# Kernel tuning notes

Measured on AMD Instinct MI355X. Metric: run time of the kernel, lower is better.

Reference implementation:

```python
import jax, jax.numpy as jnp
import numpy as np

# AdEx constants (from source module)
T_REF = 2e-3
CM = 281e-12
GL = 30e-9
EL = -70.6e-3
VT = -50.4e-3
DELTAT = 2e-3
TAUW = 144e-3
A = 4e-9
B = 0.0805e-9
DT = 1e-3
REF_STEPS = int(round(T_REF / DT))  # 2 steps


def setup_inputs() -> dict:
    key = jax.random.key(0)
    T, N = 500, 100000
    # input current ~ nanoamps so a fraction of neurons spike
    I = jax.random.normal(key, (T, N), dtype=jnp.float32) * 0.5e-9 + 0.5e-9
    v0 = jnp.full((N,), EL, dtype=jnp.float32)      # membrane potential at rest
    c0 = jnp.zeros((N,), dtype=jnp.float32)         # adaptation variable
    ref0 = jnp.zeros((N,), dtype=jnp.int32)         # refractory counters
    return {"I": I, "v0": v0, "c0": c0, "ref0": ref0}


def reference(I, v0, c0, ref0):
    """AdEx neuron simulation: scan over T timesteps, [N] state vectors.
    Returns v_trace of shape [T, N]."""

    def step(carry, I_t):
        v, c, ref = carry
        in_ref = ref > 0
        # refractory neurons are clamped to EL (tf.where(ref_op, EL, v))
        v_eff = jnp.where(in_ref, EL, v)
        # AdEx membrane dynamics (forward Euler); exp arg clipped for safety
        exp_term = GL * DELTAT * jnp.exp(jnp.minimum((v_eff - VT) / DELTAT, 15.0))
        dv = (DT / CM) * (-GL * (v_eff - EL) + exp_term - c + I_t)
        v_new = jnp.where(in_ref, EL, v_eff + dv)
        # adaptation current dynamics
        c_new = c + (DT / TAUW) * (A * (v_eff - EL) - c)
        # spike detection + reset
        spike = v_new >= VT
        v_out = jnp.where(spike, EL, v_new)
        c_out = jnp.where(spike, c_new + B, c_new)
        ref_new = jnp.where(spike, REF_STEPS, jnp.maximum(ref - 1, 0))
        return (v_out, c_out, ref_new), v_out

    (_, _, _), v_trace = jax.lax.scan(step, (v0, c0, ref0), I)
    return v_trace
```

## Files before the change

### kernel.cpp

```cpp
#include <hip/hip_runtime.h>


#define DEPTH 24

__global__ __launch_bounds__(64) void adex_kernel(
    const float* __restrict__ I,
    const float* __restrict__ v0,
    const float* __restrict__ c0,
    const int*   __restrict__ ref0,
    float*       __restrict__ out,
    int N, int T)
{
#pragma clang fp contract(off)
    const float EL       = (float)(-70.6e-3);
    const float VT       = (float)(-50.4e-3);
    const float DELTAT   = (float)(2e-3);
    const float R_DELTAT = (float)(1.0 / (double)((float)(2e-3)));
    const float NEG_GL   = (float)(-30e-9);
    const float GLDT     = (float)(30e-9 * 2e-3);
    const float DT_CM    = (float)(1e-3 / 281e-12);
    const float DT_TAUW  = (float)(1e-3 / 144e-3);
    const float Af       = (float)(4e-9);
    const float Bf       = (float)(0.0805e-9);
    const int   REF_STEPS = 2;

    int n = blockIdx.x * blockDim.x + threadIdx.x;
    if (n >= N) return;

    float v  = v0[n];
    float c  = c0[n];
    int   rf = ref0[n];

    const unsigned stride_b = (unsigned)N * 4u;

    auto step = [&](float It) -> float {
        bool  in_ref = rf > 0;
        float v_eff  = in_ref ? EL : v;

        float x   = v_eff - VT;
        float y0  = x * R_DELTAT;
        float e   = fmaf(-DELTAT, y0, x);
        float arg = fmaf(e, R_DELTAT, y0);
        arg = fminf(arg, 15.0f);
        float exp_term = GLDT * expf(arg);

        float acc = NEG_GL * (v_eff - EL);
        acc = acc + exp_term;
        acc = acc - c;
        acc = acc + It;
        float dv = DT_CM * acc;

        float v_new = in_ref ? EL : (v_eff + dv);
        float c_new = c + DT_TAUW * ((Af * (v_eff - EL)) - c);

        bool  spike = v_new >= VT;
        float v_out = spike ? EL : v_new;

        c  = spike ? (c_new + Bf) : c_new;
        rf = spike ? REF_STEPS : (in_ref ? rf - 1 : 0);
        v  = v_out;
        return v_out;
    };

    unsigned off = (unsigned)n * 4u;

    if (T >= 2 * DEPTH) {
        const char* Ip = (const char*)I + (size_t)DEPTH * (size_t)stride_b;

        float buf[DEPTH];
        {
            unsigned poff = off;
#pragma unroll
            for (int k = 0; k < DEPTH; ++k) {
                buf[k] = *(const float*)((const char*)I + poff);
                poff += stride_b;
            }
        }

        int t = 0;
        for (; t + 2 * DEPTH <= T; t += DEPTH) {
#pragma unroll
            for (int j = 0; j < DEPTH; ++j) {
                float It = buf[j];
                buf[j] = *(const float*)(Ip + off);
                float v_out = step(It);
                __builtin_nontemporal_store(v_out, (float*)((char*)out + off));
                off += stride_b;
            }
        }

#pragma unroll
        for (int j = 0; j < 2 * DEPTH; ++j) {
            if (t + j < T) {
                float It = buf[j % DEPTH];
                if (t + j + DEPTH < T) {
                    buf[j % DEPTH] = *(const float*)(Ip + off);
                }
                float v_out = step(It);
                __builtin_nontemporal_store(v_out, (float*)((char*)out + off));
                off += stride_b;
            }
        }
    } else {
        for (int tt = 0; tt < T; ++tt) {
            float It = *(const float*)((const char*)I + off);
            float v_out = step(It);
            __builtin_nontemporal_store(v_out, (float*)((char*)out + off));
            off += stride_b;
        }
    }
}

extern "C" void kernel_launch(void* const* d_in, const int* in_sizes, int n_in,
                              void* d_out, int out_size, void* d_ws, size_t ws_size,
                              hipStream_t stream) {
    const float* I    = (const float*)d_in[0];
    const float* v0   = (const float*)d_in[1];
    const float* c0   = (const float*)d_in[2];
    const int*   ref0 = (const int*)d_in[3];
    float*       out  = (float*)d_out;

    int N = in_sizes[1];
    int T = in_sizes[0] / N;

    dim3 block(64);
    dim3 grid((N + 63) / 64);
    adex_kernel<<<grid, block, 0, stream>>>(I, v0, c0, ref0, out, N, T);
}
```

Measured before the change: 363.7 us.

## Stage input tiles into LDS via async global_load_lds with double buffering

Input loads move from a per-thread register prefetch ring to 16-byte global_load_lds transfers into two LDS tiles of 32 timesteps. The next tile streams in while the current one is simulated, and the kernel reads LDS through a small register ring, synchronising with manual vmcnt waits. Partial blocks are split into a separate template path with clamped addresses. The aim is fewer VGPRs and wider, more latency-tolerant loads, but the hand-written waitcnt relies on counting outstanding memory ops (including stores) and could race or over-wait.

```diff
diff --git a/kernel.cpp b/kernel.cpp
--- a/kernel.cpp
+++ b/kernel.cpp
@@ -1,15 +1,27 @@
 #include <hip/hip_runtime.h>
 
 
-#define DEPTH 24
+#define TS 32
 
-__global__ __launch_bounds__(64) void adex_kernel(
+__device__ __forceinline__ void stage16(const void* g, void* l) {
+    __builtin_amdgcn_global_load_lds(
+        (const __attribute__((address_space(1))) void*)g,
+        (__attribute__((address_space(3))) void*)l, 16, 0, 0);
+}
+__device__ __forceinline__ void stage4(const void* g, void* l) {
+    __builtin_amdgcn_global_load_lds(
+        (const __attribute__((address_space(1))) void*)g,
+        (__attribute__((address_space(3))) void*)l, 4, 0, 0);
+}
+
+template <bool FULL>
+__device__ __forceinline__ void run_sim(
     const float* __restrict__ I,
     const float* __restrict__ v0,
     const float* __restrict__ c0,
     const int*   __restrict__ ref0,
     float*       __restrict__ out,
-    int N, int T)
+    int N, int T, float* bufA, float* bufB)
 {
 #pragma clang fp contract(off)
     const float EL       = (float)(-70.6e-3);
@@ -24,14 +36,19 @@
     const float Bf       = (float)(0.0805e-9);
     const int   REF_STEPS = 2;
 
-    int n = blockIdx.x * blockDim.x + threadIdx.x;
-    if (n >= N) return;
+    const int lane   = threadIdx.x;
+    const int n_base = blockIdx.x * 64;
+    const int n      = n_base + lane;
+    const bool active = FULL || (n < N);
+    const int  nld    = FULL ? n : (n < N ? n : N - 1);
 
-    float v  = v0[n];
-    float c  = c0[n];
-    int   rf = ref0[n];
+    float v  = v0[nld];
+    float c  = c0[nld];
+    int   rf = ref0[nld];
 
     const unsigned stride_b = (unsigned)N * 4u;
+    const char* Ic = (const char*)I;
+    char*       oc = (char*)out;
 
     auto step = [&](float It) -> float {
         bool  in_ref = rf > 0;
@@ -62,52 +79,84 @@
         return v_out;
     };
 
+    int col16 = n_base * 4 + (lane & 15) * 16;
+    if (!FULL) { int mx = N * 4 - 16; col16 = col16 < mx ? col16 : mx; }
+    const char* gst = Ic + (size_t)(lane >> 4) * stride_b + (size_t)col16;
+
+    int col4 = n * 4;
+    if (!FULL) { int mx = N * 4 - 4; col4 = col4 < mx ? col4 : mx; }
+
     unsigned off = (unsigned)n * 4u;
 
-    if (T >= 2 * DEPTH) {
-        const char* Ip = (const char*)I + (size_t)DEPTH * (size_t)stride_b;
+    const int nt = (T + TS - 1) / TS;
 
-        float buf[DEPTH];
-        {
-            unsigned poff = off;
-#pragma unroll
-            for (int k = 0; k < DEPTH; ++k) {
-                buf[k] = *(const float*)((const char*)I + poff);
-                poff += stride_b;
+    auto stage_tile = [&](int k, float* sb) {
+        int t0   = k * TS;
+        int rows = T - t0; if (rows > TS) rows = TS;
+        int full = rows >> 2;
+        for (int i = 0; i < full; ++i) {
+            stage16(gst, sb + i * 256);
+            gst += 4 * (size_t)stride_b;
+        }
+        int rem = rows & 3;
+        if (rem) {
+            const char* g4 = Ic + (size_t)(t0 + (full << 2)) * stride_b + (size_t)col4;
+            float* lb = sb + (full << 2) * 64;
+            for (int r = 0; r < rem; ++r) {
+                stage4(g4, lb);
+                g4 += stride_b; lb += 64;
             }
         }
+    };
 
-        int t = 0;
-        for (; t + 2 * DEPTH <= T; t += DEPTH) {
+    auto tile_body = [&](int k, const float* rb, float* sb) {
+        if (k + 1 < nt) stage_tile(k + 1, sb);
+
+        int rows = T - k * TS; if (rows > TS) rows = TS;
+
+        float ring[4];
 #pragma unroll
-            for (int j = 0; j < DEPTH; ++j) {
-                float It = buf[j];
-                buf[j] = *(const float*)(Ip + off);
+        for (int i = 0; i < 4; ++i)
+            if (i < rows) ring[i] = rb[i * 64 + lane];
+
+#pragma unroll
+        for (int r = 0; r < TS; ++r) {
+            if (r < rows) {
+                float It = ring[r & 3];
+                if (r + 4 < rows) ring[r & 3] = rb[(r + 4) * 64 + lane];
                 float v_out = step(It);
-                __builtin_nontemporal_store(v_out, (float*)((char*)out + off));
+                if (active)
+                    __builtin_nontemporal_store(v_out, (float*)(oc + off));
                 off += stride_b;
             }
         }
+        asm volatile("s_waitcnt vmcnt(32)" ::: "memory");
+    };
 
-#pragma unroll
-        for (int j = 0; j < 2 * DEPTH; ++j) {
-            if (t + j < T) {
-                float It = buf[j % DEPTH];
-                if (t + j + DEPTH < T) {
-                    buf[j % DEPTH] = *(const float*)(Ip + off);
-                }
-                float v_out = step(It);
-                __builtin_nontemporal_store(v_out, (float*)((char*)out + off));
-                off += stride_b;
-            }
-        }
+    stage_tile(0, bufA);
+    asm volatile("s_waitcnt vmcnt(0)" ::: "memory");
+
+    for (int k = 0; k < nt; k += 2) {
+        tile_body(k, bufA, bufB);
+        if (k + 1 < nt) tile_body(k + 1, bufB, bufA);
+    }
+}
+
+__global__ __launch_bounds__(64) void adex_kernel(
+    const float* __restrict__ I,
+    const float* __restrict__ v0,
+    const float* __restrict__ c0,
+    const int*   __restrict__ ref0,
+    float*       __restrict__ out,
+    int N, int T)
+{
+    __shared__ float bufA[TS * 64];
+    __shared__ float bufB[TS * 64];
+
+    if (blockIdx.x * 64 + 64 <= (unsigned)N) {
+        run_sim<true >(I, v0, c0, ref0, out, N, T, bufA, bufB);
     } else {
-        for (int tt = 0; tt < T; ++tt) {
-            float It = *(const float*)((const char*)I + off);
-            float v_out = step(It);
-            __builtin_nontemporal_store(v_out, (float*)((char*)out + off));
-            off += stride_b;
-        }
+        run_sim<false>(I, v0, c0, ref0, out, N, T, bufA, bufB);
     }
 }
 
```

New measurement: 400.4 us. +10.1%, slower.

## Double-buffer input prefetch in 32-step chunks with sched barriers

Applied to the files above, without the earlier changes.

Replaces the rolling 24-deep per-step prefetch ring with two 32-element register buffers that alternate. Each chunk of loads is issued ahead of the matching compute block, and scheduling barriers stop the compiler from interleaving them. It also switches from nontemporal stores to plain stores. The intent is deeper, batched memory-level parallelism, at the cost of more register use and extra predicated tail logic.

```diff
diff --git a/kernel.cpp b/kernel.cpp
--- a/kernel.cpp
+++ b/kernel.cpp
@@ -1,7 +1,7 @@
 #include <hip/hip_runtime.h>
 
 
-#define DEPTH 24
+#define TS 32
 
 __global__ __launch_bounds__(64) void adex_kernel(
     const float* __restrict__ I,
@@ -32,6 +32,10 @@
     int   rf = ref0[n];
 
     const unsigned stride_b = (unsigned)N * 4u;
+    const char* Icp = (const char*)I   + (size_t)n * 4u;
+    char*       ocp = (char*)out       + (size_t)n * 4u;
+    unsigned lo = 0;
+    unsigned so = 0;
 
     auto step = [&](float It) -> float {
         bool  in_ref = rf > 0;
@@ -62,51 +66,61 @@
         return v_out;
     };
 
-    unsigned off = (unsigned)n * 4u;
+    float A[TS], B[TS];
 
-    if (T >= 2 * DEPTH) {
-        const char* Ip = (const char*)I + (size_t)DEPTH * (size_t)stride_b;
-
-        float buf[DEPTH];
-        {
-            unsigned poff = off;
-#pragma unroll
-            for (int k = 0; k < DEPTH; ++k) {
-                buf[k] = *(const float*)((const char*)I + poff);
-                poff += stride_b;
-            }
-        }
-
-        int t = 0;
-        for (; t + 2 * DEPTH <= T; t += DEPTH) {
-#pragma unroll
-            for (int j = 0; j < DEPTH; ++j) {
-                float It = buf[j];
-                buf[j] = *(const float*)(Ip + off);
-                float v_out = step(It);
-                __builtin_nontemporal_store(v_out, (float*)((char*)out + off));
-                off += stride_b;
-            }
-        }
+    if (T >= TS) {
+        int t_done = 0;
+        int l_done = TS;
 
 #pragma unroll
-        for (int j = 0; j < 2 * DEPTH; ++j) {
-            if (t + j < T) {
-                float It = buf[j % DEPTH];
-                if (t + j + DEPTH < T) {
-                    buf[j % DEPTH] = *(const float*)(Ip + off);
-                }
-                float v_out = step(It);
-                __builtin_nontemporal_store(v_out, (float*)((char*)out + off));
-                off += stride_b;
+        for (int j = 0; j < TS; ++j) { A[j] = *(const float*)(Icp + lo); lo += stride_b; }
+        __builtin_amdgcn_sched_barrier(0);
+
+        for (;;) {
+            {
+                int nl = T - l_done; if (nl > TS) nl = TS;
+#pragma unroll
+                for (int j = 0; j < TS; ++j)
+                    if (j < nl) { B[j] = *(const float*)(Icp + lo); lo += stride_b; }
+                __builtin_amdgcn_sched_barrier(0);
+                l_done += nl;
+
+                int cnt = T - t_done; if (cnt > TS) cnt = TS;
+#pragma unroll
+                for (int j = 0; j < TS; ++j)
+                    if (j < cnt) {
+                        float vo = step(A[j]);
+                        *(float*)(ocp + so) = vo;
+                        so += stride_b;
+                    }
+                t_done += cnt;
+                if (t_done >= T) break;
+            }
+            {
+                int nl = T - l_done; if (nl > TS) nl = TS;
+#pragma unroll
+                for (int j = 0; j < TS; ++j)
+                    if (j < nl) { A[j] = *(const float*)(Icp + lo); lo += stride_b; }
+                __builtin_amdgcn_sched_barrier(0);
+                l_done += nl;
+
+                int cnt = T - t_done; if (cnt > TS) cnt = TS;
+#pragma unroll
+                for (int j = 0; j < TS; ++j)
+                    if (j < cnt) {
+                        float vo = step(B[j]);
+                        *(float*)(ocp + so) = vo;
+                        so += stride_b;
+                    }
+                t_done += cnt;
+                if (t_done >= T) break;
             }
         }
     } else {
         for (int tt = 0; tt < T; ++tt) {
-            float It = *(const float*)((const char*)I + off);
-            float v_out = step(It);
-            __builtin_nontemporal_store(v_out, (float*)((char*)out + off));
-            off += stride_b;
+            float It = *(const float*)(Icp + lo); lo += stride_b;
+            float vo = step(It);
+            *(float*)(ocp + so) = vo; so += stride_b;
         }
     }
 }
```

Result: slower. 383.6 us (+5.5%).
